# Kernel optimization log

Measured on AMD Instinct MI355X. Metric: run time of the kernel, lower is better.

Reference implementation:

```python
import jax, jax.numpy as jnp
import numpy as np

NB_STEPS = 50  # quadrature steps (51 Clenshaw-Curtis nodes)
IN_D = 8
HIDDEN = [256, 256, 256]
B = 8192


def _cc_quadrature(nb_steps):
    # Clenshaw-Curtis weights/nodes, exactly as in UMNN's ParallelNeuralIntegral
    lam = np.arange(nb_steps + 1).reshape(-1, 1)
    lam = np.cos((lam @ lam.T) * np.pi / nb_steps)
    lam[:, 0] = 0.5
    lam[:, -1] = 0.5 * lam[:, -1]
    lam = lam * 2.0 / nb_steps
    W = np.arange(nb_steps + 1).reshape(-1, 1)
    W[np.arange(1, nb_steps + 1, 2)] = 0
    W = 2.0 / (1 - W.astype(np.float64) ** 2)
    W[0] = 1.0
    W[np.arange(1, nb_steps + 1, 2)] = 0.0
    cc_weights = (lam.T @ W).astype(np.float32)  # [S+1, 1]
    steps = np.cos(np.arange(nb_steps + 1).reshape(-1, 1) * np.pi / nb_steps).astype(np.float32)  # [S+1,1]
    return jnp.asarray(cc_weights), jnp.asarray(steps)


def setup_inputs() -> dict:
    key = jax.random.key(0)
    ks = jax.random.split(key, 20)
    inp = {
        "x": jax.random.normal(ks[0], (B, 1), dtype=jnp.float32),
        "h": jax.random.normal(ks[1], (B, IN_D - 1), dtype=jnp.float32),
    }
    # integrand net: in_d -> 256 -> 256 -> 256 -> 1
    i_dims = [IN_D] + HIDDEN + [1]
    for li, (d0, d1) in enumerate(zip(i_dims, i_dims[1:])):
        scale = 1.0 / np.sqrt(d0)
        inp[f"iW{li}"] = jax.random.uniform(ks[2 + li], (d0, d1), jnp.float32, -scale, scale)
        inp[f"ib{li}"] = jax.random.uniform(ks[6 + li], (d1,), jnp.float32, -scale, scale)
    # h net: (in_d-1) -> 256 -> 256 -> 256 -> 2
    h_dims = [IN_D - 1] + HIDDEN + [2]
    for li, (d0, d1) in enumerate(zip(h_dims, h_dims[1:])):
        scale = 1.0 / np.sqrt(d0)
        inp[f"hW{li}"] = jax.random.uniform(ks[10 + li], (d0, d1), jnp.float32, -scale, scale)
        inp[f"hb{li}"] = jax.random.uniform(ks[14 + li], (d1,), jnp.float32, -scale, scale)
    return inp


def _integrand(z, Ws, bs):
    # IntegrandNN: Linear+ReLU chain, final Linear+ELU, then +1
    for W, b in zip(Ws[:-1], bs[:-1]):
        z = jax.nn.relu(z @ W + b)
    return jax.nn.elu(z @ Ws[-1] + bs[-1]) + 1.0


def _hnet(z, Ws, bs):
    # Linear+ReLU chain, final Linear (ReLU popped)
    for W, b in zip(Ws[:-1], bs[:-1]):
        z = jax.nn.relu(z @ W + b)
    return z @ Ws[-1] + bs[-1]


def _forward(x, h, iWs, ibs, hWs, hbs):
    cc_w, steps = _cc_quadrature(NB_STEPS)  # [S,1], [S,1]
    S = NB_STEPS + 1
    b = x.shape[0]
    # quadrature nodes mapped from [-1,1] to [0, x] (x0 = 0)
    X = x[:, None, :] * (steps[None, :, :] + 1.0) * 0.5          # [B,S,1]
    Hs = jnp.broadcast_to(h[:, None, :], (b, S, h.shape[1]))     # [B,S,in_d-1]
    z = jnp.concatenate([X, Hs], axis=-1)                        # [B,S,in_d]
    dz = _integrand(z, iWs, ibs)                                 # [B,S,1]
    integral = jnp.sum(dz * cc_w[None, :, :], axis=1) * x * 0.5  # [B,1]
    out = _hnet(h, hWs, hbs)                                     # [B,2]
    offset = out[:, :1]
    scaling = jnp.exp(out[:, 1:2])
    return scaling * integral + offset


def reference(x, h, iW0, ib0, iW1, ib1, iW2, ib2, iW3, ib3,
              hW0, hb0, hW1, hb1, hW2, hb2, hW3, hb3):
    iWs = [iW0, iW1, iW2, iW3]
    ibs = [ib0, ib1, ib2, ib3]
    hWs = [hW0, hW1, hW2, hW3]
    hbs = [hb0, hb1, hb2, hb3]
    return _forward(x, h, iWs, ibs, hWs, hbs)
```

## Files before the change

### kernel.cpp

```cpp
#include <hip/hip_runtime.h>
#include <hip/hip_bf16.h>
#include <math.h>

using bf16x8 = __attribute__((ext_vector_type(8))) __bf16;
using f32x4  = __attribute__((ext_vector_type(4))) float;

#define B_SZ    8192
#define S_STEPS 51
#define M_ROWS  (B_SZ * S_STEPS)

__device__ __forceinline__ f32x4 mfma16(bf16x8 a, bf16x8 b, f32x4 c) {
    return __builtin_amdgcn_mfma_f32_16x16x32_bf16(a, b, c, 0, 0, 0);
}

__global__ void ccq_kernel(float* __restrict__ ccw, float* __restrict__ stp) {
    int s = threadIdx.x;
    if (s >= S_STEPS) return;
    double pi50 = M_PI / 50.0;
    double acc = 0.0;
    for (int j = 0; j <= 50; j += 2) {
        double wq = (j == 0) ? 1.0 : 2.0 / (1.0 - (double)(j * j));
        double m;
        if (s == 0) m = 0.5;
        else if (s == 50) m = 0.5;
        else m = cos((double)(j * s) * pi50);
        acc += m * wq;
    }
    ccw[s] = (float)(acc * (2.0 / 50.0));
    stp[s] = (float)cos((double)s * pi50);
}

struct PackArgs {
    const float* src[8];
    __hip_bfloat16* dst[8];
    int Ks[8], Ns[8], KST[8], perm[8];
    int prefix[9];
};

__global__ void pack_all(PackArgs pa) {
    int idx = blockIdx.x * 256 + threadIdx.x;
    if (idx >= pa.prefix[8]) return;
    int m = 0;
    while (idx >= pa.prefix[m + 1]) ++m;
    int e = idx - pa.prefix[m];
    int KSTEPS = pa.KST[m];
    int j    = e & 7;
    int lane = (e >> 3) & 63;
    int ks   = (e >> 9) % KSTEPS;
    int cg   = (e >> 9) / KSTEPS;
    int col = cg * 16 + (lane & 15);
    int k   = ks * 32 + (lane >> 4) * 8 + j;
    int kk  = pa.perm[m] ? ((k & ~31) + ((k & 31) >> 1) + (k & 1) * 16) : k;
    float v = (kk < pa.Ks[m] && col < pa.Ns[m]) ? pa.src[m][kk * pa.Ns[m] + col] : 0.0f;
    ((__bf16*)pa.dst[m])[e] = (__bf16)v;
}


template<int KSTEPS, int CHUNKS, int MASK>
__device__ __forceinline__ void gemm_layer(const __bf16* __restrict__ actIn,
                                           const __bf16* __restrict__ wpack,
                                           const float* __restrict__ bias,
                                           __bf16* __restrict__ actOut,
                                           int wr, int wc, int lane) {
    const bf16x8* wp = (const bf16x8*)wpack;
    const int la = lane & 15, hi = lane >> 4;
    f32x4 acc[2][4];
#pragma unroll
    for (int m = 0; m < 2; ++m)
#pragma unroll
        for (int n = 0; n < 4; ++n) acc[m][n] = (f32x4)0.0f;

    bf16x8 bbuf[2][4];
#pragma unroll
    for (int n = 0; n < 4; ++n)
        bbuf[0][n] = wp[((wc * 4 + n) * KSTEPS) * 64 + lane];

#pragma unroll
    for (int ks = 0; ks < KSTEPS; ++ks) {
        bf16x8 af[2];
#pragma unroll
        for (int m = 0; m < 2; ++m) {
            int row   = wr * 32 + m * 16 + la;
            int chunk = ks * 4 + hi;
            af[m] = *(const bf16x8*)(actIn + (row * CHUNKS + (chunk ^ (row & MASK))) * 8);
        }
        if (ks + 1 < KSTEPS) {
#pragma unroll
            for (int n = 0; n < 4; ++n)
                bbuf[(ks + 1) & 1][n] = wp[((wc * 4 + n) * KSTEPS + ks + 1) * 64 + lane];
        }
#pragma unroll
        for (int m = 0; m < 2; ++m)
#pragma unroll
            for (int n = 0; n < 4; ++n)
                acc[m][n] = mfma16(af[m], bbuf[ks & 1][n], acc[m][n]);
    }
    unsigned* dst = (unsigned*)actOut;
#pragma unroll
    for (int p = 0; p < 2; ++p) {
        int f0 = wc * 64 + p * 32 + la;
        float b0 = bias[f0], b1 = bias[f0 + 16];
        int kd = (wc * 2 + p) * 16 + la;
#pragma unroll
        for (int m = 0; m < 2; ++m) {
#pragma unroll
            for (int r = 0; r < 4; ++r) {
                int row = wr * 32 + m * 16 + hi * 4 + r;
                float v0 = fmaxf(acc[m][2 * p][r] + b0, 0.0f);
                float v1 = fmaxf(acc[m][2 * p + 1][r] + b1, 0.0f);
                union { __bf16 h[2]; unsigned u; } cv;
                cv.h[0] = (__bf16)v0; cv.h[1] = (__bf16)v1;
                dst[(row * 32 + ((kd >> 2) ^ (row & 7))) * 4 + (kd & 3)] = cv.u;
            }
        }
    }
}

template<int MODE>
__device__ __forceinline__ void final_layer(const __bf16* __restrict__ actIn,
                                            const __bf16* __restrict__ wpack,
                                            const float* __restrict__ bias,
                                            float* __restrict__ out0,
                                            float* __restrict__ out1,
                                            int rb, int wid, int lane) {
    const bf16x8* wp = (const bf16x8*)wpack;
    f32x4 acc = (f32x4)0.0f;
    for (int ks = 0; ks < 8; ++ks) {
        int row   = wid * 16 + (lane & 15);
        int chunk = ks * 4 + (lane >> 4);
        bf16x8 af = *(const bf16x8*)(actIn + (row * 32 + (chunk ^ (row & 7))) * 8);
        acc = mfma16(af, wp[ks * 64 + lane], acc);
    }
    int col = lane & 15;
    if (MODE == 0) {
        if (col == 0) {
            float b = bias[0];
#pragma unroll
            for (int r = 0; r < 4; ++r) {
                int row = wid * 16 + (lane >> 4) * 4 + r;
                float v = acc[r] + b;
                out0[rb + row] = (v > 0.0f) ? (v + 1.0f) : expf(v);
            }
        }
    } else {
        if (col < 2) {
            float b = bias[col];
            float* dst = (col == 0) ? out0 : out1;
#pragma unroll
            for (int r = 0; r < 4; ++r) {
                int row = wid * 16 + (lane >> 4) * 4 + r;
                dst[rb + row] = acc[r] + b;
            }
        }
    }
}

template<int MODE>
__global__ __launch_bounds__(512) void mlp_kernel(
    const float* __restrict__ x, const float* __restrict__ h,
    const float* __restrict__ steps,
    const __bf16* __restrict__ w0p, const __bf16* __restrict__ w1p,
    const __bf16* __restrict__ w2p, const __bf16* __restrict__ w3p,
    const float* __restrict__ b0, const float* __restrict__ b1,
    const float* __restrict__ b2, const float* __restrict__ b3,
    float* __restrict__ out0, float* __restrict__ out1) {
    __shared__ __bf16 actA[64 * 256];
    __shared__ __bf16 actB[64 * 256];
    __bf16* zin = actB;

    int tid  = threadIdx.x;
    int lane = tid & 63;
    int wid  = tid >> 6;
    int wr   = wid >> 2;
    int wc   = wid & 3;
    int rb   = blockIdx.x * 64;

    if (tid < 256) {
        int row   = tid >> 2;
        int cpart = tid & 3;
        float vals[8];
        if (MODE == 0) {
            int s  = rb >> 13;
            int i  = (rb & (B_SZ - 1)) + row;
            float sc = (steps[s] + 1.0f) * 0.5f;
#pragma unroll
            for (int j = 0; j < 8; ++j) {
                int c = cpart * 8 + j;
                float v = 0.0f;
                if (c == 0) v = x[i] * sc;
                else if (c < 8) v = h[i * 7 + c - 1];
                vals[j] = v;
            }
        } else {
            int i = rb + row;
#pragma unroll
            for (int j = 0; j < 8; ++j) {
                int c = cpart * 8 + j;
                vals[j] = (c < 7) ? h[i * 7 + c] : 0.0f;
            }
        }
        bf16x8 zv;
#pragma unroll
        for (int j = 0; j < 8; ++j) zv[j] = (__bf16)vals[j];
        int zidx = (row * 4 + (cpart ^ (row & 3))) * 8;
        *(bf16x8*)(zin + zidx) = zv;
    }
    __syncthreads();

    gemm_layer<1, 4, 3>(zin, w0p, b0, actA, wr, wc, lane);
    __syncthreads();
    gemm_layer<8, 32, 7>(actA, w1p, b1, actB, wr, wc, lane);
    __syncthreads();
    gemm_layer<8, 32, 7>(actB, w2p, b2, actA, wr, wc, lane);
    __syncthreads();
    if (wid < 4)
        final_layer<MODE>(actA, w3p, b3, out0, out1, rb, wid, lane);
}

__global__ void reduce_kernel(const float* __restrict__ dz, const float* __restrict__ x,
                              const float* __restrict__ ho, const float* __restrict__ hs,
                              const float* __restrict__ ccw, float* __restrict__ out) {
    __shared__ float w[S_STEPS];
    int t = threadIdx.x;
    if (t < S_STEPS) w[t] = ccw[t];
    __syncthreads();
    int i = blockIdx.x * blockDim.x + t;
    float acc = 0.0f;
    for (int s = 0; s < S_STEPS; ++s) acc += dz[s * B_SZ + i] * w[s];
    float integral = acc * x[i] * 0.5f;
    out[i] = expf(hs[i]) * integral + ho[i];
}

extern "C" void kernel_launch(void* const* d_in, const int* in_sizes, int n_in,
                              void* d_out, int out_size, void* d_ws, size_t ws_size,
                              hipStream_t stream) {
    (void)in_sizes; (void)n_in; (void)out_size; (void)ws_size;
    const float* x = (const float*)d_in[0];
    const float* h = (const float*)d_in[1];
    const float* iW[4] = {(const float*)d_in[2], (const float*)d_in[4],
                          (const float*)d_in[6], (const float*)d_in[8]};
    const float* ib[4] = {(const float*)d_in[3], (const float*)d_in[5],
                          (const float*)d_in[7], (const float*)d_in[9]};
    const float* hW[4] = {(const float*)d_in[10], (const float*)d_in[12],
                          (const float*)d_in[14], (const float*)d_in[16]};
    const float* hb[4] = {(const float*)d_in[11], (const float*)d_in[13],
                          (const float*)d_in[15], (const float*)d_in[17]};

    size_t off = 0;
    auto alloc = [&](size_t bytes) -> void* {
        void* p = (char*)d_ws + off;
        off += (bytes + 255) & ~(size_t)255;
        return p;
    };
    float*  dz   = (float*)alloc((size_t)M_ROWS * 4);
    float*  ho   = (float*)alloc(B_SZ * 4);
    float*  hs   = (float*)alloc(B_SZ * 4);
    float*  ccw  = (float*)alloc(64 * 4);
    float*  stp  = (float*)alloc(64 * 4);
    __bf16* iW0p = (__bf16*)alloc(16 * 1 * 512 * 2);
    __bf16* iW1p = (__bf16*)alloc(16 * 8 * 512 * 2);
    __bf16* iW2p = (__bf16*)alloc(16 * 8 * 512 * 2);
    __bf16* iW3p = (__bf16*)alloc(1 * 8 * 512 * 2);
    __bf16* hW0p = (__bf16*)alloc(16 * 1 * 512 * 2);
    __bf16* hW1p = (__bf16*)alloc(16 * 8 * 512 * 2);
    __bf16* hW2p = (__bf16*)alloc(16 * 8 * 512 * 2);
    __bf16* hW3p = (__bf16*)alloc(1 * 8 * 512 * 2);

    ccq_kernel<<<1, 64, 0, stream>>>(ccw, stp);

    PackArgs pa;
    const float* srcs[8] = {iW[0], iW[1], iW[2], iW[3], hW[0], hW[1], hW[2], hW[3]};
    __bf16*      dsts[8] = {iW0p, iW1p, iW2p, iW3p, hW0p, hW1p, hW2p, hW3p};
    int Ks[8]  = {8, 256, 256, 256, 7, 256, 256, 256};
    int Ns[8]  = {256, 256, 256, 1, 256, 256, 256, 2};
    int KST[8] = {1, 8, 8, 8, 1, 8, 8, 8};
    int CG[8]  = {16, 16, 16, 1, 16, 16, 16, 1};
    int PM[8]  = {0, 1, 1, 1, 0, 1, 1, 1};
    int pfx = 0;
    for (int m = 0; m < 8; ++m) {
        pa.src[m] = srcs[m];
        pa.dst[m] = (__hip_bfloat16*)dsts[m];
        pa.Ks[m] = Ks[m]; pa.Ns[m] = Ns[m]; pa.KST[m] = KST[m]; pa.perm[m] = PM[m];
        pa.prefix[m] = pfx;
        pfx += CG[m] * KST[m] * 512;
    }
    pa.prefix[8] = pfx;
    pack_all<<<(pfx + 255) / 256, 256, 0, stream>>>(pa);

    mlp_kernel<0><<<M_ROWS / 64, 512, 0, stream>>>(
        x, h, stp, iW0p, iW1p, iW2p, iW3p, ib[0], ib[1], ib[2], ib[3], dz, dz);
    mlp_kernel<1><<<B_SZ / 64, 512, 0, stream>>>(
        x, h, stp, hW0p, hW1p, hW2p, hW3p, hb[0], hb[1], hb[2], hb[3], ho, hs);

    reduce_kernel<<<B_SZ / 256, 256, 0, stream>>>(dz, x, ho, hs, ccw, (float*)d_out);
}
```

Before: 166.4 us.

## Double row tile to 128 per block and reuse a single shared activation buffer

Each block now handles 128 rows instead of 64. Every wave computes a 64x64 output tile (4x4 MFMA accumulators) rather than 32x64, so each weight fragment loaded from global memory feeds twice as many MFMAs. Layers now write back into one shared activation buffer in place, with an extra barrier between compute and store, which keeps LDS use near 72KB per block. The costs are more accumulator registers per wave, an extra sync per layer, and half as many blocks for the small h-net launch.

Result: slower. 267.2 us (+60.6%).

```diff
diff --git a/kernel.cpp b/kernel.cpp
--- a/kernel.cpp
+++ b/kernel.cpp
@@ -8,6 +8,7 @@
 #define B_SZ    8192
 #define S_STEPS 51
 #define M_ROWS  (B_SZ * S_STEPS)
+#define TROWS   128
 
 __device__ __forceinline__ f32x4 mfma16(bf16x8 a, bf16x8 b, f32x4 c) {
     return __builtin_amdgcn_mfma_f32_16x16x32_bf16(a, b, c, 0, 0, 0);
@@ -57,18 +58,12 @@
 
 
 template<int KSTEPS, int CHUNKS, int MASK>
-__device__ __forceinline__ void gemm_layer(const __bf16* __restrict__ actIn,
-                                           const __bf16* __restrict__ wpack,
-                                           const float* __restrict__ bias,
-                                           __bf16* __restrict__ actOut,
-                                           int wr, int wc, int lane) {
+__device__ __forceinline__ void gemm_compute(const __bf16* __restrict__ actIn,
+                                             const __bf16* __restrict__ wpack,
+                                             f32x4 (&acc)[4][4],
+                                             int wr, int wc, int lane) {
     const bf16x8* wp = (const bf16x8*)wpack;
     const int la = lane & 15, hi = lane >> 4;
-    f32x4 acc[2][4];
-#pragma unroll
-    for (int m = 0; m < 2; ++m)
-#pragma unroll
-        for (int n = 0; n < 4; ++n) acc[m][n] = (f32x4)0.0f;
 
     bf16x8 bbuf[2][4];
 #pragma unroll
@@ -77,10 +72,10 @@
 
 #pragma unroll
     for (int ks = 0; ks < KSTEPS; ++ks) {
-        bf16x8 af[2];
-#pragma unroll
-        for (int m = 0; m < 2; ++m) {
-            int row   = wr * 32 + m * 16 + la;
+        bf16x8 af[4];
+#pragma unroll
+        for (int m = 0; m < 4; ++m) {
+            int row   = wr * 64 + m * 16 + la;
             int chunk = ks * 4 + hi;
             af[m] = *(const bf16x8*)(actIn + (row * CHUNKS + (chunk ^ (row & MASK))) * 8);
         }
@@ -90,11 +85,18 @@
                 bbuf[(ks + 1) & 1][n] = wp[((wc * 4 + n) * KSTEPS + ks + 1) * 64 + lane];
         }
 #pragma unroll
-        for (int m = 0; m < 2; ++m)
+        for (int m = 0; m < 4; ++m)
 #pragma unroll
             for (int n = 0; n < 4; ++n)
                 acc[m][n] = mfma16(af[m], bbuf[ks & 1][n], acc[m][n]);
     }
+}
+
+__device__ __forceinline__ void epilogue_store(f32x4 (&acc)[4][4],
+                                               const float* __restrict__ bias,
+                                               __bf16* __restrict__ actOut,
+                                               int wr, int wc, int lane) {
+    const int la = lane & 15, hi = lane >> 4;
     unsigned* dst = (unsigned*)actOut;
 #pragma unroll
     for (int p = 0; p < 2; ++p) {
@@ -102,10 +104,10 @@
         float b0 = bias[f0], b1 = bias[f0 + 16];
         int kd = (wc * 2 + p) * 16 + la;
 #pragma unroll
-        for (int m = 0; m < 2; ++m) {
+        for (int m = 0; m < 4; ++m) {
 #pragma unroll
             for (int r = 0; r < 4; ++r) {
-                int row = wr * 32 + m * 16 + hi * 4 + r;
+                int row = wr * 64 + m * 16 + hi * 4 + r;
                 float v0 = fmaxf(acc[m][2 * p][r] + b0, 0.0f);
                 float v1 = fmaxf(acc[m][2 * p + 1][r] + b1, 0.0f);
                 union { __bf16 h[2]; unsigned u; } cv;
@@ -156,7 +158,7 @@
 }
 
 template<int MODE>
-__global__ __launch_bounds__(512) void mlp_kernel(
+__global__ __launch_bounds__(512, 4) void mlp_kernel(
     const float* __restrict__ x, const float* __restrict__ h,
     const float* __restrict__ steps,
     const __bf16* __restrict__ w0p, const __bf16* __restrict__ w1p,
@@ -164,18 +166,17 @@
     const float* __restrict__ b0, const float* __restrict__ b1,
     const float* __restrict__ b2, const float* __restrict__ b3,
     float* __restrict__ out0, float* __restrict__ out1) {
-    __shared__ __bf16 actA[64 * 256];
-    __shared__ __bf16 actB[64 * 256];
-    __bf16* zin = actB;
+    __shared__ __bf16 act[TROWS * 256];
+    __shared__ __bf16 zin[TROWS * 32];
 
     int tid  = threadIdx.x;
     int lane = tid & 63;
     int wid  = tid >> 6;
     int wr   = wid >> 2;
     int wc   = wid & 3;
-    int rb   = blockIdx.x * 64;
-
-    if (tid < 256) {
+    int rb   = blockIdx.x * TROWS;
+
+    {
         int row   = tid >> 2;
         int cpart = tid & 3;
         float vals[8];
@@ -207,14 +208,35 @@
     }
     __syncthreads();
 
-    gemm_layer<1, 4, 3>(zin, w0p, b0, actA, wr, wc, lane);
-    __syncthreads();
-    gemm_layer<8, 32, 7>(actA, w1p, b1, actB, wr, wc, lane);
-    __syncthreads();
-    gemm_layer<8, 32, 7>(actB, w2p, b2, actA, wr, wc, lane);
-    __syncthreads();
-    if (wid < 4)
-        final_layer<MODE>(actA, w3p, b3, out0, out1, rb, wid, lane);
+    f32x4 acc[4][4];
+
+#pragma unroll
+    for (int m = 0; m < 4; ++m)
+#pragma unroll
+        for (int n = 0; n < 4; ++n) acc[m][n] = (f32x4)0.0f;
+    gemm_compute<1, 4, 3>(zin, w0p, acc, wr, wc, lane);
+    epilogue_store(acc, b0, act, wr, wc, lane);
+    __syncthreads();
+
+#pragma unroll
+    for (int m = 0; m < 4; ++m)
+#pragma unroll
+        for (int n = 0; n < 4; ++n) acc[m][n] = (f32x4)0.0f;
+    gemm_compute<8, 32, 7>(act, w1p, acc, wr, wc, lane);
+    __syncthreads();
+    epilogue_store(acc, b1, act, wr, wc, lane);
+    __syncthreads();
+
+#pragma unroll
+    for (int m = 0; m < 4; ++m)
+#pragma unroll
+        for (int n = 0; n < 4; ++n) acc[m][n] = (f32x4)0.0f;
+    gemm_compute<8, 32, 7>(act, w2p, acc, wr, wc, lane);
+    __syncthreads();
+    epilogue_store(acc, b2, act, wr, wc, lane);
+    __syncthreads();
+
+    final_layer<MODE>(act, w3p, b3, out0, out1, rb, wid, lane);
 }
 
 __global__ void reduce_kernel(const float* __restrict__ dz, const float* __restrict__ x,
@@ -287,9 +309,9 @@
     pa.prefix[8] = pfx;
     pack_all<<<(pfx + 255) / 256, 256, 0, stream>>>(pa);
 
-    mlp_kernel<0><<<M_ROWS / 64, 512, 0, stream>>>(
+    mlp_kernel<0><<<M_ROWS / TROWS, 512, 0, stream>>>(
         x, h, stp, iW0p, iW1p, iW2p, iW3p, ib[0], ib[1], ib[2], ib[3], dz, dz);
-    mlp_kernel<1><<<B_SZ / 64, 512, 0, stream>>>(
+    mlp_kernel<1><<<B_SZ / TROWS, 512, 0, stream>>>(
         x, h, stp, hW0p, hW1p, hW2p, hW3p, hb[0], hb[1], hb[2], hb[3], ho, hs);
 
     reduce_kernel<<<B_SZ / 256, 256, 0, stream>>>(dz, x, ho, hs, ccw, (float*)d_out);
```
